# Performance work log

Measured on AMD Instinct MI355X. Metric: run time of the kernel, lower is better.

Reference implementation:

```python
import jax, jax.numpy as jnp
import numpy as np


def setup_inputs() -> dict:
    key = jax.random.key(0)
    k1, k2 = jax.random.split(key)
    B, C, H, W = 16, 256, 64, 64
    return {
        "x1": jax.random.normal(k1, (B, C, H, W), dtype=jnp.float32),
        "x2": jax.random.normal(k2, (B, C, H, W), dtype=jnp.float32),
        "k": 256,
    }


def reference(x1, x2, k):
    # concat along channels: [B, 2C, H, W]
    x = jnp.concatenate([x1, x2], axis=1)
    # adaptive avgpool to (1,1) == global mean over H,W -> [B, C_tot]
    pooled = jnp.mean(x, axis=(2, 3))
    # torch.topk(pooled, num_channels) == full descending sort indices
    idx = jnp.argsort(-pooled, axis=1)  # [B, C_tot]
    # gather channels in descending pooled-mean order
    xr = jnp.take_along_axis(x, idx[:, :, None, None], axis=1)  # [B, C_tot, H, W]
    # sum trailing channels [k:] and fold into channel k-1
    tail = jnp.sum(xr[:, k:, :, :], axis=1)  # [B, H, W]
    out = xr[:, :k, :, :].at[:, k - 1, :, :].add(tail)
    return out
```

## Files before the change

### kernel.cpp

```cpp
#include <hip/hip_runtime.h>

#define B   16
#define C1  256
#define C2  512
#define HW  4096
#define TCHUNK 32

typedef float vf4 __attribute__((ext_vector_type(4)));

__device__ __forceinline__ const vf4* chan_base(
    const float* __restrict__ x1, const float* __restrict__ x2, int b, int c)
{
    return (const vf4*)((c < C1) ? (x1 + (size_t)(b * C1 + c) * HW)
                                 : (x2 + (size_t)(b * C1 + (c - C1)) * HW));
}

__global__ __launch_bounds__(256) void reduce_kernel(
    const float* __restrict__ x1, const float* __restrict__ x2,
    float* __restrict__ total,
    float* __restrict__ partials)
{
    int bid   = blockIdx.x;
    int b     = bid / TCHUNK;
    int chunk = bid % TCHUNK;
    int t     = threadIdx.x;
    int g     = t >> 5;
    int slot  = t & 31;
    int off   = chunk * 32 + slot;

    float* pp = partials + (size_t)(b * TCHUNK + chunk) * C2;

    vf4 t0 = (vf4)(0.f), t1 = (vf4)(0.f), t2 = (vf4)(0.f), t3 = (vf4)(0.f);

    for (int j = 0; j < 64; j += 4) {
        int c0 = (j + 0) * 8 + g, c1 = (j + 1) * 8 + g;
        int c2 = (j + 2) * 8 + g, c3 = (j + 3) * 8 + g;
        vf4 v0 = chan_base(x1, x2, b, c0)[off];
        vf4 v1 = chan_base(x1, x2, b, c1)[off];
        vf4 v2 = chan_base(x1, x2, b, c2)[off];
        vf4 v3 = chan_base(x1, x2, b, c3)[off];
        t0 += v0; t1 += v1; t2 += v2; t3 += v3;

        float h0 = (v0.x + v0.y) + (v0.z + v0.w);
        float h1 = (v1.x + v1.y) + (v1.z + v1.w);
        float h2 = (v2.x + v2.y) + (v2.z + v2.w);
        float h3 = (v3.x + v3.y) + (v3.z + v3.w);
        #pragma unroll
        for (int s = 16; s > 0; s >>= 1) {
            h0 += __shfl_down(h0, s, 32);
            h1 += __shfl_down(h1, s, 32);
            h2 += __shfl_down(h2, s, 32);
            h3 += __shfl_down(h3, s, 32);
        }
        if (slot == 0) {
            pp[c0] = h0; pp[c1] = h1; pp[c2] = h2; pp[c3] = h3;
        }
    }

    __shared__ vf4 red[8][32];
    red[g][slot] = (t0 + t1) + (t2 + t3);
    __syncthreads();
    if (g == 0) {
        vf4 r = (vf4)(0.f);
        #pragma unroll
        for (int gg = 0; gg < 8; ++gg)
            r += red[gg][slot];
        ((vf4*)(total + (size_t)b * HW))[off] = r;
    }
}

__global__ __launch_bounds__(512) void sort_kernel(
    const float* __restrict__ partials, int* __restrict__ idx)
{
    int b = blockIdx.x;
    int t = threadIdx.x;
    const float* pp = partials + (size_t)b * TCHUNK * C2 + t;
    float v = 0.f;
    #pragma unroll
    for (int ch = 0; ch < TCHUNK; ++ch)
        v += pp[ch * C2];

    __shared__ float sp[C2];
    sp[t] = v;
    __syncthreads();
    int rank = 0;
    for (int j = 0; j < C2; ++j) {
        float u = sp[j];
        rank += (u > v) || (u == v && j < t);
    }
    idx[b * C2 + rank] = t;
}

__global__ __launch_bounds__(256) void output_kernel(
    const float* __restrict__ x1, const float* __restrict__ x2,
    const int* __restrict__ idx, const float* __restrict__ total,
    float* __restrict__ out, int k)
{
    int bid   = blockIdx.x;
    int b     = bid / TCHUNK;
    int chunk = bid % TCHUNK;
    int t     = threadIdx.x;
    int g     = t >> 5;
    int slot  = t & 31;
    int off   = chunk * 32 + slot;
    int nh    = k - 1;

    __shared__ int ch[C2 / 2];
    __shared__ vf4 red[8][32];
    for (int i = t; i < nh; i += 256)
        ch[i] = idx[b * C2 + i];
    __syncthreads();

    vf4 a0 = (vf4)(0.f), a1 = (vf4)(0.f), a2 = (vf4)(0.f), a3 = (vf4)(0.f);
    const size_t ob = (size_t)b * k;
    int r = g;
    for (; r + 24 < nh; r += 32) {
        int c0 = ch[r], c1 = ch[r + 8], c2 = ch[r + 16], c3 = ch[r + 24];
        vf4 v0 = chan_base(x1, x2, b, c0)[off];
        vf4 v1 = chan_base(x1, x2, b, c1)[off];
        vf4 v2 = chan_base(x1, x2, b, c2)[off];
        vf4 v3 = chan_base(x1, x2, b, c3)[off];
        ((vf4*)(out + (ob + r     ) * HW))[off] = v0;
        ((vf4*)(out + (ob + r +  8) * HW))[off] = v1;
        ((vf4*)(out + (ob + r + 16) * HW))[off] = v2;
        ((vf4*)(out + (ob + r + 24) * HW))[off] = v3;
        a0 += v0; a1 += v1; a2 += v2; a3 += v3;
    }
    for (; r < nh; r += 8) {
        int c0 = ch[r];
        vf4 v0 = chan_base(x1, x2, b, c0)[off];
        ((vf4*)(out + (ob + r) * HW))[off] = v0;
        a0 += v0;
    }

    red[g][slot] = (a0 + a1) + (a2 + a3);
    __syncthreads();
    if (g == 0) {
        vf4 hsum = (vf4)(0.f);
        #pragma unroll
        for (int gg = 0; gg < 8; ++gg)
            hsum += red[gg][slot];
        vf4 tt = ((const vf4*)(total + (size_t)b * HW))[off];
        ((vf4*)(out + (ob + (k - 1)) * HW))[off] = tt - hsum;
    }
}

extern "C" void kernel_launch(void* const* d_in, const int* in_sizes, int n_in,
                              void* d_out, int out_size, void* d_ws, size_t ws_size,
                              hipStream_t stream)
{
    const float* x1 = (const float*)d_in[0];
    const float* x2 = (const float*)d_in[1];
    float* out = (float*)d_out;

    int k = out_size / (B * HW);

    int*   idx      = (int*)d_ws;
    float* total    = (float*)((char*)d_ws + B * C2 * sizeof(int));
    float* partials = total + (size_t)B * HW;

    reduce_kernel<<<B * TCHUNK, 256, 0, stream>>>(x1, x2, total, partials);
    sort_kernel<<<B, 512, 0, stream>>>(partials, idx);
    output_kernel<<<B * TCHUNK, 256, 0, stream>>>(x1, x2, idx, total, out, k);
}
```

Baseline: 63.90 us.

## Fuse reduce, sort and gather kernels into one cooperative kernel with grid sync

```diff
diff --git a/kernel.cpp b/kernel.cpp
--- a/kernel.cpp
+++ b/kernel.cpp
@@ -1,4 +1,7 @@
 #include <hip/hip_runtime.h>
+#include <hip/hip_cooperative_groups.h>
+
+namespace cg = cooperative_groups;
 
 #define B   16
 #define C1  256
@@ -15,11 +18,13 @@
                                  : (x2 + (size_t)(b * C1 + (c - C1)) * HW));
 }
 
-__global__ __launch_bounds__(256) void reduce_kernel(
+__global__ __launch_bounds__(256) void fused_kernel(
     const float* __restrict__ x1, const float* __restrict__ x2,
-    float* __restrict__ total,
-    float* __restrict__ partials)
+    float* __restrict__ partials,
+    float* __restrict__ out, int k)
 {
+    cg::grid_group grid = cg::this_grid();
+
     int bid   = blockIdx.x;
     int b     = bid / TCHUNK;
     int chunk = bid % TCHUNK;
@@ -28,8 +33,11 @@
     int slot  = t & 31;
     int off   = chunk * 32 + slot;
 
+    __shared__ vf4   red[8][32];
+    __shared__ float sp[C2];
+    __shared__ int   idxl[C2];
+
     float* pp = partials + (size_t)(b * TCHUNK + chunk) * C2;
-
     vf4 t0 = (vf4)(0.f), t1 = (vf4)(0.f), t2 = (vf4)(0.f), t3 = (vf4)(0.f);
 
     for (int j = 0; j < 64; j += 4) {
@@ -57,65 +65,46 @@
         }
     }
 
-    __shared__ vf4 red[8][32];
     red[g][slot] = (t0 + t1) + (t2 + t3);
     __syncthreads();
+    vf4 tt = (vf4)(0.f);
     if (g == 0) {
-        vf4 r = (vf4)(0.f);
         #pragma unroll
         for (int gg = 0; gg < 8; ++gg)
-            r += red[gg][slot];
-        ((vf4*)(total + (size_t)b * HW))[off] = r;
+            tt += red[gg][slot];
     }
-}
 
-__global__ __launch_bounds__(512) void sort_kernel(
-    const float* __restrict__ partials, int* __restrict__ idx)
-{
-    int b = blockIdx.x;
-    int t = threadIdx.x;
-    const float* pp = partials + (size_t)b * TCHUNK * C2 + t;
-    float v = 0.f;
-    #pragma unroll
-    for (int ch = 0; ch < TCHUNK; ++ch)
-        v += pp[ch * C2];
+    __threadfence();
+    grid.sync();
 
-    __shared__ float sp[C2];
-    sp[t] = v;
-    __syncthreads();
-    int rank = 0;
-    for (int j = 0; j < C2; ++j) {
-        float u = sp[j];
-        rank += (u > v) || (u == v && j < t);
+    {
+        int cA = t, cB = t + 256;
+        const float* pb = partials + (size_t)b * TCHUNK * C2;
+        float vA = 0.f, vB = 0.f;
+        #pragma unroll
+        for (int ch = 0; ch < TCHUNK; ++ch) {
+            vA += pb[ch * C2 + cA];
+            vB += pb[ch * C2 + cB];
+        }
+        sp[cA] = vA; sp[cB] = vB;
+        __syncthreads();
+        int rA = 0, rB = 0;
+        for (int j = 0; j < C2; ++j) {
+            float u = sp[j];
+            rA += (u > vA) || (u == vA && j < cA);
+            rB += (u > vB) || (u == vB && j < cB);
+        }
+        idxl[rA] = cA;
+        idxl[rB] = cB;
+        __syncthreads();
     }
-    idx[b * C2 + rank] = t;
-}
 
-__global__ __launch_bounds__(256) void output_kernel(
-    const float* __restrict__ x1, const float* __restrict__ x2,
-    const int* __restrict__ idx, const float* __restrict__ total,
-    float* __restrict__ out, int k)
-{
-    int bid   = blockIdx.x;
-    int b     = bid / TCHUNK;
-    int chunk = bid % TCHUNK;
-    int t     = threadIdx.x;
-    int g     = t >> 5;
-    int slot  = t & 31;
-    int off   = chunk * 32 + slot;
-    int nh    = k - 1;
-
-    __shared__ int ch[C2 / 2];
-    __shared__ vf4 red[8][32];
-    for (int i = t; i < nh; i += 256)
-        ch[i] = idx[b * C2 + i];
-    __syncthreads();
-
+    int nh = k - 1;
     vf4 a0 = (vf4)(0.f), a1 = (vf4)(0.f), a2 = (vf4)(0.f), a3 = (vf4)(0.f);
     const size_t ob = (size_t)b * k;
     int r = g;
     for (; r + 24 < nh; r += 32) {
-        int c0 = ch[r], c1 = ch[r + 8], c2 = ch[r + 16], c3 = ch[r + 24];
+        int c0 = idxl[r], c1 = idxl[r + 8], c2 = idxl[r + 16], c3 = idxl[r + 24];
         vf4 v0 = chan_base(x1, x2, b, c0)[off];
         vf4 v1 = chan_base(x1, x2, b, c1)[off];
         vf4 v2 = chan_base(x1, x2, b, c2)[off];
@@ -127,12 +116,13 @@
         a0 += v0; a1 += v1; a2 += v2; a3 += v3;
     }
     for (; r < nh; r += 8) {
-        int c0 = ch[r];
+        int c0 = idxl[r];
         vf4 v0 = chan_base(x1, x2, b, c0)[off];
         ((vf4*)(out + (ob + r) * HW))[off] = v0;
         a0 += v0;
     }
 
+    __syncthreads();
     red[g][slot] = (a0 + a1) + (a2 + a3);
     __syncthreads();
     if (g == 0) {
@@ -140,7 +130,6 @@
         #pragma unroll
         for (int gg = 0; gg < 8; ++gg)
             hsum += red[gg][slot];
-        vf4 tt = ((const vf4*)(total + (size_t)b * HW))[off];
         ((vf4*)(out + (ob + (k - 1)) * HW))[off] = tt - hsum;
     }
 }
@@ -155,11 +144,11 @@
 
     int k = out_size / (B * HW);
 
-    int*   idx      = (int*)d_ws;
-    float* total    = (float*)((char*)d_ws + B * C2 * sizeof(int));
-    float* partials = total + (size_t)B * HW;
+    float* partials = (float*)d_ws;
 
-    reduce_kernel<<<B * TCHUNK, 256, 0, stream>>>(x1, x2, total, partials);
-    sort_kernel<<<B, 512, 0, stream>>>(partials, idx);
-    output_kernel<<<B * TCHUNK, 256, 0, stream>>>(x1, x2, idx, total, out, k);
+    void* args[] = { (void*)&x1, (void*)&x2, (void*)&partials,
+                     (void*)&out, (void*)&k };
+    hipLaunchCooperativeKernel((const void*)fused_kernel,
+                               dim3(B * TCHUNK), dim3(256),
+                               args, 0, stream);
 }
```

After: 173.8 us. 172% more time.

## Fuse sort into output kernel and reduce contiguous channel slabs

Applied to the files above, without the earlier changes.

```diff
diff --git a/kernel.cpp b/kernel.cpp
--- a/kernel.cpp
+++ b/kernel.cpp
@@ -4,6 +4,7 @@
 #define C1  256
 #define C2  512
 #define HW  4096
+#define NSLAB 32
 #define TCHUNK 32
 
 typedef float vf4 __attribute__((ext_vector_type(4)));
@@ -15,10 +16,132 @@
                                  : (x2 + (size_t)(b * C1 + (c - C1)) * HW));
 }
 
-__global__ __launch_bounds__(256) void reduce_kernel(
-    const float* __restrict__ x1, const float* __restrict__ x2,
-    float* __restrict__ total,
-    float* __restrict__ partials)
+__global__ __launch_bounds__(256) void slab_reduce_kernel(
+    const float* __restrict__ x1, const float* __restrict__ x2,
+    float* __restrict__ pooled,
+    float* __restrict__ pixpart)
+{
+    int bid = blockIdx.x;
+    int b   = bid >> 5;
+    int s   = bid & 31;
+    int t   = threadIdx.x;
+
+    const float* base = (s < 16)
+        ? x1 + ((size_t)b * C1 + s * 16) * HW
+        : x2 + ((size_t)b * C1 + (s - 16) * 16) * HW;
+    const vf4* p = (const vf4*)base;
+
+    vf4 px0 = (vf4)(0.f), px1 = px0, px2 = px0, px3 = px0;
+    float h[16];
+    #pragma unroll
+    for (int j = 0; j < 16; ++j) h[j] = 0.f;
+
+    #pragma unroll
+    for (int j = 0; j < 16; ++j) {
+        vf4 v0 = p[j * 1024 + t];
+        vf4 v1 = p[j * 1024 + t + 256];
+        vf4 v2 = p[j * 1024 + t + 512];
+        vf4 v3 = p[j * 1024 + t + 768];
+        px0 += v0; px1 += v1; px2 += v2; px3 += v3;
+        h[j] += ((v0.x + v0.y) + (v0.z + v0.w))
+              + ((v1.x + v1.y) + (v1.z + v1.w))
+              + ((v2.x + v2.y) + (v2.z + v2.w))
+              + ((v3.x + v3.y) + (v3.z + v3.w));
+    }
+
+    vf4* pp = (vf4*)(pixpart + ((size_t)b * NSLAB + s) * HW);
+    pp[t] = px0; pp[t + 256] = px1; pp[t + 512] = px2; pp[t + 768] = px3;
+
+    __shared__ float hacc[16][258];
+    #pragma unroll
+    for (int j = 0; j < 16; ++j) hacc[j][t] = h[j];
+    __syncthreads();
+    if (t < 16) {
+        float sum = 0.f;
+        for (int i = 0; i < 256; ++i) sum += hacc[t][i];
+        pooled[b * C2 + s * 16 + t] = sum;
+    }
+}
+
+__global__ __launch_bounds__(256) void output2_kernel(
+    const float* __restrict__ x1, const float* __restrict__ x2,
+    const float* __restrict__ pooled, const float* __restrict__ pixpart,
+    float* __restrict__ out, int k)
+{
+    int bid   = blockIdx.x;
+    int b     = bid >> 5;
+    int chunk = bid & 31;
+    int t     = threadIdx.x;
+    int g     = t >> 5;
+    int slot  = t & 31;
+    int off   = chunk * 32 + slot;
+
+    __shared__ float sp[C2];
+    __shared__ int   idxl[C2];
+    __shared__ vf4   red[8][32];
+
+    {
+        int cA = t, cB = t + 256;
+        float vA = pooled[b * C2 + cA];
+        float vB = pooled[b * C2 + cB];
+        sp[cA] = vA; sp[cB] = vB;
+        __syncthreads();
+        int rA = 0, rB = 0;
+        for (int j = 0; j < C2; ++j) {
+            float u = sp[j];
+            rA += (u > vA) || (u == vA && j < cA);
+            rB += (u > vB) || (u == vB && j < cB);
+        }
+        idxl[rA] = cA;
+        idxl[rB] = cB;
+        __syncthreads();
+    }
+
+    int nh = k - 1;
+    vf4 a0 = (vf4)(0.f), a1 = (vf4)(0.f), a2 = (vf4)(0.f), a3 = (vf4)(0.f);
+    const size_t ob = (size_t)b * k;
+    int r = g;
+    for (; r + 24 < nh; r += 32) {
+        int c0 = idxl[r], c1 = idxl[r + 8], c2 = idxl[r + 16], c3 = idxl[r + 24];
+        vf4 v0 = chan_base(x1, x2, b, c0)[off];
+        vf4 v1 = chan_base(x1, x2, b, c1)[off];
+        vf4 v2 = chan_base(x1, x2, b, c2)[off];
+        vf4 v3 = chan_base(x1, x2, b, c3)[off];
+        ((vf4*)(out + (ob + r     ) * HW))[off] = v0;
+        ((vf4*)(out + (ob + r +  8) * HW))[off] = v1;
+        ((vf4*)(out + (ob + r + 16) * HW))[off] = v2;
+        ((vf4*)(out + (ob + r + 24) * HW))[off] = v3;
+        a0 += v0; a1 += v1; a2 += v2; a3 += v3;
+    }
+    for (; r < nh; r += 8) {
+        int c0 = idxl[r];
+        vf4 v0 = chan_base(x1, x2, b, c0)[off];
+        ((vf4*)(out + (ob + r) * HW))[off] = v0;
+        a0 += v0;
+    }
+
+    vf4 tp = (vf4)(0.f);
+    {
+        const vf4* pb = (const vf4*)(pixpart + (size_t)b * NSLAB * HW);
+        #pragma unroll
+        for (int m = 0; m < 4; ++m)
+            tp += pb[(size_t)(g + m * 8) * 1024 + off];
+    }
+
+    red[g][slot] = tp - ((a0 + a1) + (a2 + a3));
+    __syncthreads();
+    if (g == 0) {
+        vf4 res = (vf4)(0.f);
+        #pragma unroll
+        for (int gg = 0; gg < 8; ++gg)
+            res += red[gg][slot];
+        ((vf4*)(out + (ob + (k - 1)) * HW))[off] = res;
+    }
+}
+
+__global__ __launch_bounds__(256) void fb_reduce_kernel(
+    const float* __restrict__ x1, const float* __restrict__ x2,
+    float* __restrict__ total, float* __restrict__ partials)
 {
     int bid   = blockIdx.x;
     int b     = bid / TCHUNK;
@@ -29,7 +152,6 @@
     int off   = chunk * 32 + slot;
 
     float* pp = partials + (size_t)(b * TCHUNK + chunk) * C2;
-
     vf4 t0 = (vf4)(0.f), t1 = (vf4)(0.f), t2 = (vf4)(0.f), t3 = (vf4)(0.f);
 
     for (int j = 0; j < 64; j += 4) {
@@ -40,7 +162,6 @@
         vf4 v2 = chan_base(x1, x2, b, c2)[off];
         vf4 v3 = chan_base(x1, x2, b, c3)[off];
         t0 += v0; t1 += v1; t2 += v2; t3 += v3;
-
         float h0 = (v0.x + v0.y) + (v0.z + v0.w);
         float h1 = (v1.x + v1.y) + (v1.z + v1.w);
         float h2 = (v2.x + v2.y) + (v2.z + v2.w);
@@ -52,9 +173,7 @@
             h2 += __shfl_down(h2, s, 32);
             h3 += __shfl_down(h3, s, 32);
         }
-        if (slot == 0) {
-            pp[c0] = h0; pp[c1] = h1; pp[c2] = h2; pp[c3] = h3;
-        }
+        if (slot == 0) { pp[c0] = h0; pp[c1] = h1; pp[c2] = h2; pp[c3] = h3; }
     }
 
     __shared__ vf4 red[8][32];
@@ -63,13 +182,12 @@
     if (g == 0) {
         vf4 r = (vf4)(0.f);
         #pragma unroll
-        for (int gg = 0; gg < 8; ++gg)
-            r += red[gg][slot];
+        for (int gg = 0; gg < 8; ++gg) r += red[gg][slot];
         ((vf4*)(total + (size_t)b * HW))[off] = r;
     }
 }
 
-__global__ __launch_bounds__(512) void sort_kernel(
+__global__ __launch_bounds__(512) void fb_sort_kernel(
     const float* __restrict__ partials, int* __restrict__ idx)
 {
     int b = blockIdx.x;
@@ -77,9 +195,7 @@
     const float* pp = partials + (size_t)b * TCHUNK * C2 + t;
     float v = 0.f;
     #pragma unroll
-    for (int ch = 0; ch < TCHUNK; ++ch)
-        v += pp[ch * C2];
-
+    for (int ch = 0; ch < TCHUNK; ++ch) v += pp[ch * C2];
     __shared__ float sp[C2];
     sp[t] = v;
     __syncthreads();
@@ -91,7 +207,7 @@
     idx[b * C2 + rank] = t;
 }
 
-__global__ __launch_bounds__(256) void output_kernel(
+__global__ __launch_bounds__(256) void fb_output_kernel(
     const float* __restrict__ x1, const float* __restrict__ x2,
     const int* __restrict__ idx, const float* __restrict__ total,
     float* __restrict__ out, int k)
@@ -107,8 +223,7 @@
 
     __shared__ int ch[C2 / 2];
     __shared__ vf4 red[8][32];
-    for (int i = t; i < nh; i += 256)
-        ch[i] = idx[b * C2 + i];
+    for (int i = t; i < nh; i += 256) ch[i] = idx[b * C2 + i];
     __syncthreads();
 
     vf4 a0 = (vf4)(0.f), a1 = (vf4)(0.f), a2 = (vf4)(0.f), a3 = (vf4)(0.f);
@@ -138,8 +253,7 @@
     if (g == 0) {
         vf4 hsum = (vf4)(0.f);
         #pragma unroll
-        for (int gg = 0; gg < 8; ++gg)
-            hsum += red[gg][slot];
+        for (int gg = 0; gg < 8; ++gg) hsum += red[gg][slot];
         vf4 tt = ((const vf4*)(total + (size_t)b * HW))[off];
         ((vf4*)(out + (ob + (k - 1)) * HW))[off] = tt - hsum;
     }
@@ -155,11 +269,20 @@
 
     int k = out_size / (B * HW);
 
-    int*   idx      = (int*)d_ws;
-    float* total    = (float*)((char*)d_ws + B * C2 * sizeof(int));
-    float* partials = total + (size_t)B * HW;
-
-    reduce_kernel<<<B * TCHUNK, 256, 0, stream>>>(x1, x2, total, partials);
-    sort_kernel<<<B, 512, 0, stream>>>(partials, idx);
-    output_kernel<<<B * TCHUNK, 256, 0, stream>>>(x1, x2, idx, total, out, k);
-}
+    size_t need_fast = (size_t)B * C2 * sizeof(float)
+                     + (size_t)B * NSLAB * HW * sizeof(float);
+
+    if (ws_size >= need_fast) {
+        float* pooled  = (float*)d_ws;
+        float* pixpart = pooled + B * C2;
+        slab_reduce_kernel<<<B * NSLAB, 256, 0, stream>>>(x1, x2, pooled, pixpart);
+        output2_kernel<<<B * TCHUNK, 256, 0, stream>>>(x1, x2, pooled, pixpart, out, k);
+    } else {
+        int*   idx      = (int*)d_ws;
+        float* total    = (float*)((char*)d_ws + B * C2 * sizeof(int));
+        float* partials = total + (size_t)B * HW;
+        fb_reduce_kernel<<<B * TCHUNK, 256, 0, stream>>>(x1, x2, total, partials);
+        fb_sort_kernel<<<B, 512, 0, stream>>>(partials, idx);
+        fb_output_kernel<<<B * TCHUNK, 256, 0, stream>>>(x1, x2, idx, total, out, k);
+    }
+}
```

After: 70.92 us. 11.0% more time.
